# Performance work log

Measured on AMD Instinct MI355X. Metric: run time of the kernel, lower is better.

Reference implementation:

```python
import jax, jax.numpy as jnp
import numpy as np

D_MODEL = 1024
N_HEAD = 16


def setup_inputs() -> dict:
    key = jax.random.key(0)
    ks = jax.random.split(key, 7)
    B, L, D = 2, 2048, D_MODEL
    s = 0.02
    return {
        "x": jax.random.normal(ks[0], (B, L, D), dtype=jnp.float32),
        "W_kq": jax.random.normal(ks[1], (D, 2 * D), dtype=jnp.float32) * s,
        "b_kq": jax.random.normal(ks[2], (2 * D,), dtype=jnp.float32) * s,
        "W_v": jax.random.normal(ks[3], (D, D), dtype=jnp.float32) * s,
        "b_v": jax.random.normal(ks[4], (D,), dtype=jnp.float32) * s,
        "W_o": jax.random.normal(ks[5], (D, D), dtype=jnp.float32) * s,
        "b_o": jax.random.normal(ks[6], (D,), dtype=jnp.float32) * s,
    }


def reference(x, W_kq, b_kq, W_v, b_v, W_o, b_o):
    B, L, D = x.shape
    H = N_HEAD
    dh = D // H
    kq = x @ W_kq + b_kq            # (B, L, 2D); split order: k first, then q
    k = kq[..., :D].reshape(B, L, H, dh)
    q = kq[..., D:].reshape(B, L, H, dh)
    v = (x @ W_v + b_v).reshape(B, L, H, dh)
    scale = 1.0 / jnp.sqrt(jnp.float32(dh))
    scores = jnp.einsum('blhd,bmhd->bhlm', q, k) * scale  # (B, H, L, L)
    causal = jnp.tril(jnp.ones((L, L), dtype=bool))
    scores = jnp.where(causal, scores, -jnp.inf)
    attn = jax.nn.softmax(scores, axis=-1)
    out = jnp.einsum('bhlm,bmhd->blhd', attn, v).reshape(B, L, D)
    out = out @ W_o + b_o
    return jnp.squeeze(out)
```

## Files before the change

### kernel.cpp

```cpp
#include <hip/hip_runtime.h>
#include <cstdint>


#define LSEQ 2048
#define DM   1024
#define BL   4096

using frag_ab = __attribute__((ext_vector_type(8))) short;
using half8   = __attribute__((ext_vector_type(8))) _Float16;
using half4   = __attribute__((ext_vector_type(4))) _Float16;
using f32x4   = __attribute__((ext_vector_type(4))) float;

__device__ __forceinline__ unsigned short f2bf(float f) {
  unsigned int u = __float_as_uint(f);
  u += 0x7fffu + ((u >> 16) & 1u);
  return (unsigned short)(u >> 16);
}

__device__ __forceinline__ void load_lds16(const void* g, void* l) {
  __builtin_amdgcn_global_load_lds(
      (const __attribute__((address_space(1))) unsigned int*)g,
      (__attribute__((address_space(3))) unsigned int*)l, 16, 0, 0);
}


__global__ __launch_bounds__(256) void cast_bf16_kernel(
    const float* __restrict__ in, unsigned short* __restrict__ out, int n4)
{
  int i = (blockIdx.x * 256 + threadIdx.x);
  if (i < n4) {
    const float4 v = *(const float4*)&in[i * 4];
    ushort4 o;
    o.x = f2bf(v.x); o.y = f2bf(v.y); o.z = f2bf(v.z); o.w = f2bf(v.w);
    *(ushort4*)&out[i * 4] = o;
  }
}

__global__ __launch_bounds__(256) void transpose_cast_kernel(
    const float* __restrict__ W, unsigned short* __restrict__ Wt, int K, int N)
{
  __shared__ float tile[32][33];
  const int r  = threadIdx.x >> 3;
  const int c4 = (threadIdx.x & 7) * 4;
  const int kb = blockIdx.y * 32;
  const int nb = blockIdx.x * 32;

  const float4 v = *(const float4*)&W[(size_t)(kb + r) * N + nb + c4];
  tile[r][c4 + 0] = v.x; tile[r][c4 + 1] = v.y;
  tile[r][c4 + 2] = v.z; tile[r][c4 + 3] = v.w;
  __syncthreads();
  ushort4 o;
  o.x = f2bf(tile[c4 + 0][r]);
  o.y = f2bf(tile[c4 + 1][r]);
  o.z = f2bf(tile[c4 + 2][r]);
  o.w = f2bf(tile[c4 + 3][r]);
  *(ushort4*)&Wt[(size_t)(nb + r) * K + kb + c4] = o;
}

__global__ __launch_bounds__(256) void transpose_cast_f16_kernel(
    const float* __restrict__ W, _Float16* __restrict__ Wt, int K, int N)
{
  __shared__ float tile[32][33];
  const int r  = threadIdx.x >> 3;
  const int c4 = (threadIdx.x & 7) * 4;
  const int kb = blockIdx.y * 32;
  const int nb = blockIdx.x * 32;

  const float4 v = *(const float4*)&W[(size_t)(kb + r) * N + nb + c4];
  tile[r][c4 + 0] = v.x; tile[r][c4 + 1] = v.y;
  tile[r][c4 + 2] = v.z; tile[r][c4 + 3] = v.w;
  __syncthreads();
  half4 o;
  o[0] = (_Float16)tile[c4 + 0][r];
  o[1] = (_Float16)tile[c4 + 1][r];
  o[2] = (_Float16)tile[c4 + 2][r];
  o[3] = (_Float16)tile[c4 + 3][r];
  *(half4*)&Wt[(size_t)(nb + r) * K + kb + c4] = o;
}


__global__ __launch_bounds__(256) void gemm_kqv(
    const unsigned short* __restrict__ A, const unsigned short* __restrict__ Bt,
    const float* __restrict__ b_kq, const float* __restrict__ b_v,
    unsigned short* __restrict__ kqb, _Float16* __restrict__ vtb)
{
  const int tid  = threadIdx.x;
  const int lane = tid & 63;
  const int w    = tid >> 6;
  const int wm   = (w >> 1) * 64;
  const int wn   = (w & 1) * 64;
  const int n0   = blockIdx.x * 128;
  const int m0   = blockIdx.y * 128;
  const int quad = lane >> 4;
  const int l15  = lane & 15;
  const int K    = 1024;

  __shared__ __align__(16) unsigned short As[128 * 64];
  __shared__ __align__(16) unsigned short Bs[128 * 64];

  const int srow = lane >> 3;
  const int sc   = (lane & 7) ^ srow;

  const unsigned short* gA = A  + (size_t)(m0 + w * 32 + srow) * K + sc * 8;
  const unsigned short* gB = Bt + (size_t)(n0 + w * 32 + srow) * K + sc * 8;

  f32x4 acc[4][4] = {};

  for (int k0 = 0; k0 < K; k0 += 64) {
    __syncthreads();
#pragma unroll
    for (int i = 0; i < 4; ++i) {
      load_lds16(gA + (size_t)i * 8 * K + k0, &As[(w * 32 + i * 8) * 64 + lane * 8]);
      load_lds16(gB + (size_t)i * 8 * K + k0, &Bs[(w * 32 + i * 8) * 64 + lane * 8]);
    }
    __syncthreads();
#pragma unroll
    for (int kf = 0; kf < 2; ++kf) {
      frag_ab af[4], bf[4];
#pragma unroll
      for (int t = 0; t < 4; ++t) {
        const int ra = wm + t * 16 + l15;
        const int pa = (kf * 4 + quad) ^ (ra & 7);
        af[t] = *(const frag_ab*)&As[ra * 64 + pa * 8];
        const int rb = wn + t * 16 + l15;
        const int pb = (kf * 4 + quad) ^ (rb & 7);
        bf[t] = *(const frag_ab*)&Bs[rb * 64 + pb * 8];
      }
#pragma unroll
      for (int i = 0; i < 4; ++i)
#pragma unroll
        for (int j = 0; j < 4; ++j)
          acc[i][j] = __builtin_amdgcn_mfma_f32_16x16x32_bf16(
              af[i], bf[j], acc[i][j], 0, 0, 0);
    }
  }

  if (n0 >= 2048) {
#pragma unroll
    for (int i = 0; i < 4; ++i)
#pragma unroll
      for (int j = 0; j < 4; ++j) {
        const int row0 = m0 + wm + i * 16 + quad * 4;
        const int col  = n0 - 2048 + wn + j * 16 + l15;
        const float bv = b_v[col];
        half4 pk;
        pk[0] = (_Float16)(acc[i][j][0] + bv);
        pk[1] = (_Float16)(acc[i][j][1] + bv);
        pk[2] = (_Float16)(acc[i][j][2] + bv);
        pk[3] = (_Float16)(acc[i][j][3] + bv);
        *(half4*)&vtb[(size_t)col * BL + row0] = pk;
      }
  } else {
    const float sc2 = (n0 + wn >= 1024) ? 0.125f : 1.0f;
#pragma unroll
    for (int i = 0; i < 4; ++i)
#pragma unroll
      for (int j = 0; j < 4; ++j) {
        const int row0 = m0 + wm + i * 16 + quad * 4;
        const int col  = n0 + wn + j * 16 + l15;
        const float bv = b_kq[col];
#pragma unroll
        for (int r = 0; r < 4; ++r)
          kqb[(size_t)(row0 + r) * 2048 + col] = f2bf((acc[i][j][r] + bv) * sc2);
      }
  }
}


__global__ __launch_bounds__(256) void gemm_out(
    const _Float16* __restrict__ A, const _Float16* __restrict__ Bt,
    const float* __restrict__ bias, float* __restrict__ C)
{
  const int tid  = threadIdx.x;
  const int lane = tid & 63;
  const int w    = tid >> 6;
  const int wm   = (w >> 1) * 64;
  const int wn   = (w & 1) * 64;
  const int n0   = blockIdx.x * 128;
  const int m0   = blockIdx.y * 128;
  const int quad = lane >> 4;
  const int l15  = lane & 15;
  const int K    = 1024;

  __shared__ __align__(16) _Float16 As[128 * 64];
  __shared__ __align__(16) _Float16 Bs[128 * 64];

  const int srow = lane >> 3;
  const int sc   = (lane & 7) ^ srow;

  const _Float16* gA = A  + (size_t)(m0 + w * 32 + srow) * K + sc * 8;
  const _Float16* gB = Bt + (size_t)(n0 + w * 32 + srow) * K + sc * 8;

  f32x4 acc[4][4] = {};

  for (int k0 = 0; k0 < K; k0 += 64) {
    __syncthreads();
#pragma unroll
    for (int i = 0; i < 4; ++i) {
      load_lds16(gA + (size_t)i * 8 * K + k0, &As[(w * 32 + i * 8) * 64 + lane * 8]);
      load_lds16(gB + (size_t)i * 8 * K + k0, &Bs[(w * 32 + i * 8) * 64 + lane * 8]);
    }
    __syncthreads();
#pragma unroll
    for (int kf = 0; kf < 2; ++kf) {
      half8 af[4], bf[4];
#pragma unroll
      for (int t = 0; t < 4; ++t) {
        const int ra = wm + t * 16 + l15;
        const int pa = (kf * 4 + quad) ^ (ra & 7);
        af[t] = *(const half8*)&As[ra * 64 + pa * 8];
        const int rb = wn + t * 16 + l15;
        const int pb = (kf * 4 + quad) ^ (rb & 7);
        bf[t] = *(const half8*)&Bs[rb * 64 + pb * 8];
      }
#pragma unroll
      for (int i = 0; i < 4; ++i)
#pragma unroll
        for (int j = 0; j < 4; ++j)
          acc[i][j] = __builtin_amdgcn_mfma_f32_16x16x32_f16(
              af[i], bf[j], acc[i][j], 0, 0, 0);
    }
  }

#pragma unroll
  for (int i = 0; i < 4; ++i)
#pragma unroll
    for (int j = 0; j < 4; ++j) {
      const int row0 = m0 + wm + i * 16 + quad * 4;
      const int col  = n0 + wn + j * 16 + l15;
      const float bv = bias[col];
#pragma unroll
      for (int r = 0; r < 4; ++r)
        C[(size_t)(row0 + r) * DM + col] = acc[i][j][r] + bv;
    }
}


__global__ __launch_bounds__(256) void attn_mfma(
    const unsigned short* __restrict__ kq, const _Float16* __restrict__ vt,
    _Float16* __restrict__ att)
{
  const int tid  = threadIdx.x;
  const int lane = tid & 63;
  const int w    = tid >> 6;
  const int bx   = blockIdx.x;
  const int qt   = 31 - (bx >> 5);
  const int bh   = bx & 31;
  const int b    = bh >> 4;
  const int h    = bh & 15;
  const int q0   = qt * 64;
  const int quad = lane >> 4;
  const int l15  = lane & 15;

  __shared__ __align__(16) unsigned short Ks[128 * 64];
  __shared__ __align__(16) _Float16      Vs[64 * 128];

#pragma unroll
  for (int i = 0; i < 2; ++i) {
    const int L = i * 256 + tid;
    const int row = L >> 3, c = L & 7;
    const unsigned short* g = kq + (size_t)(b * LSEQ + q0 + row) * 2048
                                 + DM + h * 64 + ((c ^ (row & 7)) * 8);
    load_lds16(g, &Ks[(size_t)L * 8]);
  }
  __syncthreads();
  frag_ab qa[2];
#pragma unroll
  for (int kf = 0; kf < 2; ++kf) {
    const int row = w * 16 + l15;
    const int c = (kf * 4 + quad) ^ (row & 7);
    qa[kf] = *(const frag_ab*)&Ks[row * 64 + c * 8];
  }

  f32x4 oacc[4] = {};
  float mrow = -3e38f, lrow = 0.f;
  const int nk = (qt + 2) >> 1;

  for (int kt = 0; kt < nk; ++kt) {
    const int k0 = kt * 128;
    __syncthreads();
#pragma unroll
    for (int i = 0; i < 4; ++i) {
      const int L = i * 256 + tid;
      {
        const int row = L >> 3, c = L & 7;
        const unsigned short* g = kq + (size_t)(b * LSEQ + k0 + row) * 2048
                                     + h * 64 + ((c ^ (row & 7)) * 8);
        load_lds16(g, &Ks[(size_t)L * 8]);
      }
      {
        const int row = L >> 4, c16 = L & 15;
        const _Float16* g = vt + (size_t)(h * 64 + row) * BL
                               + b * LSEQ + k0 + ((c16 ^ (row & 15)) * 8);
        load_lds16(g, &Vs[(size_t)L * 8]);
      }
    }
    __syncthreads();

    f32x4 st[8];
#pragma unroll
    for (int mt = 0; mt < 8; ++mt) {
      f32x4 s = {};
#pragma unroll
      for (int kf = 0; kf < 2; ++kf) {
        const int row = mt * 16 + l15;
        const int c = (kf * 4 + quad) ^ (row & 7);
        const frag_ab kfrag = *(const frag_ab*)&Ks[row * 64 + c * 8];
        s = __builtin_amdgcn_mfma_f32_16x16x32_bf16(kfrag, qa[kf], s, 0, 0, 0);
      }
      st[mt] = s;
    }

    if (kt == nk - 1) {
      const int qg = q0 + w * 16 + l15;
#pragma unroll
      for (int mt = 0; mt < 8; ++mt)
#pragma unroll
        for (int r = 0; r < 4; ++r)
          if (k0 + mt * 16 + quad * 4 + r > qg) st[mt][r] = -3e38f;
    }

    float mx = -3e38f;
#pragma unroll
    for (int mt = 0; mt < 8; ++mt)
#pragma unroll
      for (int r = 0; r < 4; ++r) mx = fmaxf(mx, st[mt][r]);
    mx = fmaxf(mx, __shfl_xor(mx, 16));
    mx = fmaxf(mx, __shfl_xor(mx, 32));
    const float mnew  = fmaxf(mrow, mx);
    const float alpha = __expf(mrow - mnew);
    float rsum = 0.f;
#pragma unroll
    for (int mt = 0; mt < 8; ++mt)
#pragma unroll
      for (int r = 0; r < 4; ++r) {
        const float e = __expf(st[mt][r] - mnew);
        st[mt][r] = e;
        rsum += e;
      }
    rsum += __shfl_xor(rsum, 16);
    rsum += __shfl_xor(rsum, 32);
    lrow = lrow * alpha + rsum;
    mrow = mnew;

    float aq[4];
#pragma unroll
    for (int r = 0; r < 4; ++r) aq[r] = __shfl(alpha, quad * 4 + r);
#pragma unroll
    for (int dt = 0; dt < 4; ++dt)
#pragma unroll
      for (int r = 0; r < 4; ++r) oacc[dt][r] *= aq[r];

#pragma unroll
    for (int c8 = 0; c8 < 8; ++c8) {
      half4 pf;
      pf[0] = (_Float16)st[c8][0];
      pf[1] = (_Float16)st[c8][1];
      pf[2] = (_Float16)st[c8][2];
      pf[3] = (_Float16)st[c8][3];
#pragma unroll
      for (int dt = 0; dt < 4; ++dt) {
        const int g16 = 2 * c8 + (quad >> 1);
        const half4 vf = *(const half4*)&Vs[(dt * 16 + l15) * 128
                                            + ((g16 ^ l15) << 3) + ((quad & 1) << 2)];
        oacc[dt] = __builtin_amdgcn_mfma_f32_16x16x16f16(pf, vf, oacc[dt], 0, 0, 0);
      }
    }
  }

  float lq[4];
#pragma unroll
  for (int r = 0; r < 4; ++r) lq[r] = 1.0f / __shfl(lrow, quad * 4 + r);
#pragma unroll
  for (int dt = 0; dt < 4; ++dt)
#pragma unroll
    for (int r = 0; r < 4; ++r) {
      const int row = b * LSEQ + q0 + w * 16 + quad * 4 + r;
      const int col = h * 64 + dt * 16 + l15;
      att[(size_t)row * DM + col] = (_Float16)(oacc[dt][r] * lq[r]);
    }
}


extern "C" void kernel_launch(void* const* d_in, const int* in_sizes, int n_in,
                              void* d_out, int out_size, void* d_ws, size_t ws_size,
                              hipStream_t stream)
{
  const float* x    = (const float*)d_in[0];
  const float* W_kq = (const float*)d_in[1];
  const float* b_kq = (const float*)d_in[2];
  const float* W_v  = (const float*)d_in[3];
  const float* b_v  = (const float*)d_in[4];
  const float* W_o  = (const float*)d_in[5];
  const float* b_o  = (const float*)d_in[6];

  unsigned short* ws   = (unsigned short*)d_ws;
  unsigned short* xb   = ws;
  unsigned short* wcat = xb   + 4194304;
  _Float16*       wot  = (_Float16*)(wcat + 3145728);
  unsigned short* kqb  = (unsigned short*)(wot + 1048576);
  _Float16*       vtb  = (_Float16*)(kqb + 8388608);
  _Float16*       attb = vtb + 4194304;

  cast_bf16_kernel<<<4096, 256, 0, stream>>>(x, xb, 1048576);
  transpose_cast_kernel<<<dim3(64, 32), 256, 0, stream>>>(W_kq, wcat, 1024, 2048);
  transpose_cast_kernel<<<dim3(32, 32), 256, 0, stream>>>(W_v, wcat + 2097152, 1024, 1024);
  transpose_cast_f16_kernel<<<dim3(32, 32), 256, 0, stream>>>(W_o, wot, 1024, 1024);

  gemm_kqv<<<dim3(24, 32), 256, 0, stream>>>(xb, wcat, b_kq, b_v, kqb, vtb);
  attn_mfma<<<1024, 256, 0, stream>>>(kqb, vtb, attb);
  gemm_out<<<dim3(8, 32), 256, 0, stream>>>(attb, wot, b_o, (float*)d_out);
}
```

Measured before the change: 197.3 us.

## Merge prep kernels into one launch and shrink output GEMM tile width

Fuses the x cast and three weight transpose-cast kernels into a single prep_kernel, dispatched by block index, to remove three launches and their gaps. The output GEMM tile narrows from 128x128 to 128x64, doubling the grid to 512 blocks so the GPU's many CUs are better filled, at the cost of more A-tile reloads. Occupancy hints are added to launch_bounds for gemm_out and attn_mfma, which may force register limits and spilling.

```diff
diff --git a/kernel.cpp b/kernel.cpp
--- a/kernel.cpp
+++ b/kernel.cpp
@@ -24,58 +24,62 @@
 }
 
 
-__global__ __launch_bounds__(256) void cast_bf16_kernel(
-    const float* __restrict__ in, unsigned short* __restrict__ out, int n4)
+__global__ __launch_bounds__(256) void prep_kernel(
+    const float* __restrict__ x, unsigned short* __restrict__ xb,
+    const float* __restrict__ W_kq, const float* __restrict__ W_v,
+    const float* __restrict__ W_o,
+    unsigned short* __restrict__ wcat, _Float16* __restrict__ wot)
 {
-  int i = (blockIdx.x * 256 + threadIdx.x);
-  if (i < n4) {
-    const float4 v = *(const float4*)&in[i * 4];
+  const int bid = blockIdx.x;
+  const int tid = threadIdx.x;
+
+  if (bid < 4096) {
+    const int i = bid * 256 + tid;
+    const float4 v = *(const float4*)&x[(size_t)i * 4];
     ushort4 o;
     o.x = f2bf(v.x); o.y = f2bf(v.y); o.z = f2bf(v.z); o.w = f2bf(v.w);
-    *(ushort4*)&out[i * 4] = o;
-  }
-}
-
-__global__ __launch_bounds__(256) void transpose_cast_kernel(
-    const float* __restrict__ W, unsigned short* __restrict__ Wt, int K, int N)
-{
+    *(ushort4*)&xb[(size_t)i * 4] = o;
+    return;
+  }
+
   __shared__ float tile[32][33];
-  const int r  = threadIdx.x >> 3;
-  const int c4 = (threadIdx.x & 7) * 4;
-  const int kb = blockIdx.y * 32;
-  const int nb = blockIdx.x * 32;
+  const int r  = tid >> 3;
+  const int c4 = (tid & 7) * 4;
+
+  const float* W;
+  int N, nb, kb, which;
+  if (bid < 6144) {
+    const int b2 = bid - 4096;
+    W = W_kq; N = 2048; nb = (b2 & 63) * 32; kb = (b2 >> 6) * 32; which = 0;
+  } else if (bid < 7168) {
+    const int b2 = bid - 6144;
+    W = W_v;  N = 1024; nb = (b2 & 31) * 32; kb = (b2 >> 5) * 32; which = 1;
+  } else {
+    const int b2 = bid - 7168;
+    W = W_o;  N = 1024; nb = (b2 & 31) * 32; kb = (b2 >> 5) * 32; which = 2;
+  }
 
   const float4 v = *(const float4*)&W[(size_t)(kb + r) * N + nb + c4];
   tile[r][c4 + 0] = v.x; tile[r][c4 + 1] = v.y;
   tile[r][c4 + 2] = v.z; tile[r][c4 + 3] = v.w;
   __syncthreads();
-  ushort4 o;
-  o.x = f2bf(tile[c4 + 0][r]);
-  o.y = f2bf(tile[c4 + 1][r]);
-  o.z = f2bf(tile[c4 + 2][r]);
-  o.w = f2bf(tile[c4 + 3][r]);
-  *(ushort4*)&Wt[(size_t)(nb + r) * K + kb + c4] = o;
-}
-
-__global__ __launch_bounds__(256) void transpose_cast_f16_kernel(
-    const float* __restrict__ W, _Float16* __restrict__ Wt, int K, int N)
-{
-  __shared__ float tile[32][33];
-  const int r  = threadIdx.x >> 3;
-  const int c4 = (threadIdx.x & 7) * 4;
-  const int kb = blockIdx.y * 32;
-  const int nb = blockIdx.x * 32;
-
-  const float4 v = *(const float4*)&W[(size_t)(kb + r) * N + nb + c4];
-  tile[r][c4 + 0] = v.x; tile[r][c4 + 1] = v.y;
-  tile[r][c4 + 2] = v.z; tile[r][c4 + 3] = v.w;
-  __syncthreads();
-  half4 o;
-  o[0] = (_Float16)tile[c4 + 0][r];
-  o[1] = (_Float16)tile[c4 + 1][r];
-  o[2] = (_Float16)tile[c4 + 2][r];
-  o[3] = (_Float16)tile[c4 + 3][r];
-  *(half4*)&Wt[(size_t)(nb + r) * K + kb + c4] = o;
+
+  if (which == 2) {
+    half4 o;
+    o[0] = (_Float16)tile[c4 + 0][r];
+    o[1] = (_Float16)tile[c4 + 1][r];
+    o[2] = (_Float16)tile[c4 + 2][r];
+    o[3] = (_Float16)tile[c4 + 3][r];
+    *(half4*)&wot[(size_t)(nb + r) * 1024 + kb + c4] = o;
+  } else {
+    ushort4 o;
+    o.x = f2bf(tile[c4 + 0][r]);
+    o.y = f2bf(tile[c4 + 1][r]);
+    o.z = f2bf(tile[c4 + 2][r]);
+    o.w = f2bf(tile[c4 + 3][r]);
+    unsigned short* dst = (which == 0) ? wcat : wcat + 2097152;
+    *(ushort4*)&dst[(size_t)(nb + r) * 1024 + kb + c4] = o;
+  }
 }
 
 
@@ -167,7 +171,7 @@
 }
 
 
-__global__ __launch_bounds__(256) void gemm_out(
+__global__ __launch_bounds__(256, 4) void gemm_out(
     const _Float16* __restrict__ A, const _Float16* __restrict__ Bt,
     const float* __restrict__ bias, float* __restrict__ C)
 {
@@ -175,40 +179,44 @@
   const int lane = tid & 63;
   const int w    = tid >> 6;
   const int wm   = (w >> 1) * 64;
-  const int wn   = (w & 1) * 64;
-  const int n0   = blockIdx.x * 128;
+  const int wn   = (w & 1) * 32;
+  const int n0   = blockIdx.x * 64;
   const int m0   = blockIdx.y * 128;
   const int quad = lane >> 4;
   const int l15  = lane & 15;
   const int K    = 1024;
 
   __shared__ __align__(16) _Float16 As[128 * 64];
-  __shared__ __align__(16) _Float16 Bs[128 * 64];
+  __shared__ __align__(16) _Float16 Bs[64 * 64];
 
   const int srow = lane >> 3;
   const int sc   = (lane & 7) ^ srow;
 
   const _Float16* gA = A  + (size_t)(m0 + w * 32 + srow) * K + sc * 8;
-  const _Float16* gB = Bt + (size_t)(n0 + w * 32 + srow) * K + sc * 8;
-
-  f32x4 acc[4][4] = {};
+  const _Float16* gB = Bt + (size_t)(n0 + w * 16 + srow) * K + sc * 8;
+
+  f32x4 acc[4][2] = {};
 
   for (int k0 = 0; k0 < K; k0 += 64) {
     __syncthreads();
 #pragma unroll
-    for (int i = 0; i < 4; ++i) {
+    for (int i = 0; i < 4; ++i)
       load_lds16(gA + (size_t)i * 8 * K + k0, &As[(w * 32 + i * 8) * 64 + lane * 8]);
-      load_lds16(gB + (size_t)i * 8 * K + k0, &Bs[(w * 32 + i * 8) * 64 + lane * 8]);
-    }
+#pragma unroll
+    for (int i = 0; i < 2; ++i)
+      load_lds16(gB + (size_t)i * 8 * K + k0, &Bs[(w * 16 + i * 8) * 64 + lane * 8]);
     __syncthreads();
 #pragma unroll
     for (int kf = 0; kf < 2; ++kf) {
-      half8 af[4], bf[4];
+      half8 af[4], bf[2];
 #pragma unroll
       for (int t = 0; t < 4; ++t) {
         const int ra = wm + t * 16 + l15;
         const int pa = (kf * 4 + quad) ^ (ra & 7);
         af[t] = *(const half8*)&As[ra * 64 + pa * 8];
+      }
+#pragma unroll
+      for (int t = 0; t < 2; ++t) {
         const int rb = wn + t * 16 + l15;
         const int pb = (kf * 4 + quad) ^ (rb & 7);
         bf[t] = *(const half8*)&Bs[rb * 64 + pb * 8];
@@ -216,7 +224,7 @@
 #pragma unroll
       for (int i = 0; i < 4; ++i)
 #pragma unroll
-        for (int j = 0; j < 4; ++j)
+        for (int j = 0; j < 2; ++j)
           acc[i][j] = __builtin_amdgcn_mfma_f32_16x16x32_f16(
               af[i], bf[j], acc[i][j], 0, 0, 0);
     }
@@ -225,7 +233,7 @@
 #pragma unroll
   for (int i = 0; i < 4; ++i)
 #pragma unroll
-    for (int j = 0; j < 4; ++j) {
+    for (int j = 0; j < 2; ++j) {
       const int row0 = m0 + wm + i * 16 + quad * 4;
       const int col  = n0 + wn + j * 16 + l15;
       const float bv = bias[col];
@@ -236,7 +244,7 @@
 }
 
 
-__global__ __launch_bounds__(256) void attn_mfma(
+__global__ __launch_bounds__(256, 5) void attn_mfma(
     const unsigned short* __restrict__ kq, const _Float16* __restrict__ vt,
     _Float16* __restrict__ att)
 {
@@ -402,12 +410,8 @@
   _Float16*       vtb  = (_Float16*)(kqb + 8388608);
   _Float16*       attb = vtb + 4194304;
 
-  cast_bf16_kernel<<<4096, 256, 0, stream>>>(x, xb, 1048576);
-  transpose_cast_kernel<<<dim3(64, 32), 256, 0, stream>>>(W_kq, wcat, 1024, 2048);
-  transpose_cast_kernel<<<dim3(32, 32), 256, 0, stream>>>(W_v, wcat + 2097152, 1024, 1024);
-  transpose_cast_f16_kernel<<<dim3(32, 32), 256, 0, stream>>>(W_o, wot, 1024, 1024);
-
+  prep_kernel<<<8192, 256, 0, stream>>>(x, xb, W_kq, W_v, W_o, wcat, wot);
   gemm_kqv<<<dim3(24, 32), 256, 0, stream>>>(xb, wcat, b_kq, b_v, kqb, vtb);
   attn_mfma<<<1024, 256, 0, stream>>>(kqb, vtb, attb);
-  gemm_out<<<dim3(8, 32), 256, 0, stream>>>(attb, wot, b_o, (float*)d_out);
-}
+  gemm_out<<<dim3(16, 32), 256, 0, stream>>>(attb, wot, b_o, (float*)d_out);
+}
```

Result: slower. 217.6 us (+10.3%).
